# Kernel tuning notes

Hardware: AMD Instinct MI355X
Metric: run time of the kernel (lower is better)

The kernel has to match this reference:

```python
import jax, jax.numpy as jnp
import numpy as np

N = 8192
D_IN = 128
D_OUT = 128


def setup_inputs() -> dict:
    key = jax.random.key(0)
    k1, k2, k3 = jax.random.split(key, 3)
    node_features = jax.random.normal(k1, (N, D_IN), dtype=jnp.float32)
    adj_matrix = jax.random.uniform(k2, (N, N), dtype=jnp.float32)
    # Xavier-uniform weight, zero bias (as in reset_parameters)
    limit = float(np.sqrt(6.0 / (D_IN + D_OUT)))
    weight = jax.random.uniform(k3, (D_IN, D_OUT), dtype=jnp.float32,
                                minval=-limit, maxval=limit)
    bias = jnp.zeros((D_OUT,), dtype=jnp.float32)
    return {"node_features": node_features, "adj_matrix": adj_matrix,
            "weight": weight, "bias": bias}


def reference(node_features, adj_matrix, weight, bias):
    n = adj_matrix.shape[0]
    # A_hat = A + I
    a_hat = adj_matrix + jnp.eye(n, dtype=adj_matrix.dtype)
    d_hat = jnp.sum(a_hat, axis=1)  # [N]
    # pow(d, -0.5) with inf (d==0) masked to 0
    d_inv_sqrt = jnp.where(d_hat > 0, jax.lax.rsqrt(d_hat), 0.0)
    # diag(d) @ A_hat @ diag(d) == row/col broadcast scaling (same math)
    adj_normalized = d_inv_sqrt[:, None] * a_hat * d_inv_sqrt[None, :]
    support = node_features @ weight  # [N, D_OUT]
    out = adj_normalized @ support + bias
    return out
```

## Files before the change

### kernel.cpp

```cpp
#include <hip/hip_runtime.h>

#define NN 8192
#define DD 128

typedef short s16x4 __attribute__((ext_vector_type(4)));
typedef short s16x8 __attribute__((ext_vector_type(8)));
typedef float f32x4 __attribute__((ext_vector_type(4)));
typedef unsigned short u16;
typedef const void __attribute__((address_space(1))) gvoid;
typedef void __attribute__((address_space(3))) lvoid;

__device__ __forceinline__ u16 f2bf(float f) {
  unsigned int u = __float_as_uint(f);
  u += 0x7fffu + ((u >> 16) & 1u);
  return (u16)(u >> 16);
}
__device__ __forceinline__ float bf2f(u16 h) {
  return __uint_as_float(((unsigned int)h) << 16);
}

__global__ __launch_bounds__(256) void k_prep(const float* __restrict__ A,
                                              float* __restrict__ dinv,
                                              u16* __restrict__ Abf) {
  const int row = blockIdx.x;
  const float4* Ar = (const float4*)(A + (size_t)row * NN);
  ushort4* Br = (ushort4*)(Abf + (size_t)row * NN);
  const int t = threadIdx.x;
  float s = 0.f;
#pragma unroll
  for (int i = 0; i < 8; ++i) {
    float4 v = Ar[t + 256 * i];
    s += (v.x + v.y) + (v.z + v.w);
    ushort4 b;
    b.x = f2bf(v.x); b.y = f2bf(v.y); b.z = f2bf(v.z); b.w = f2bf(v.w);
    Br[t + 256 * i] = b;
  }
#pragma unroll
  for (int off = 32; off > 0; off >>= 1) s += __shfl_down(s, off, 64);
  __shared__ float red[4];
  if ((t & 63) == 0) red[t >> 6] = s;
  __syncthreads();
  if (t == 0) {
    float d = 1.0f + ((red[0] + red[1]) + (red[2] + red[3]));
    dinv[row] = d > 0.f ? rsqrtf(d) : 0.f;
  }
}

__global__ __launch_bounds__(256) void k_support(const float* __restrict__ X,
                                                 const float* __restrict__ W,
                                                 const float* __restrict__ dinv,
                                                 u16* __restrict__ tT) {
  __shared__ __align__(16) u16 Wt[128][136];
  __shared__ __align__(16) u16 Xs[32][136];
  const int t = threadIdx.x;
  const int j0 = blockIdx.x * 32;

  const float4* W4 = (const float4*)W;
#pragma unroll
  for (int s = 0; s < 16; ++s) {
    int c = t + 256 * s;
    int k = c >> 5, n4 = c & 31;
    float4 wv = W4[c];
    Wt[n4 * 4 + 0][k] = f2bf(wv.x);
    Wt[n4 * 4 + 1][k] = f2bf(wv.y);
    Wt[n4 * 4 + 2][k] = f2bf(wv.z);
    Wt[n4 * 4 + 3][k] = f2bf(wv.w);
  }
  const float4* X4 = (const float4*)(X + (size_t)j0 * DD);
#pragma unroll
  for (int s = 0; s < 4; ++s) {
    int c = t + 256 * s;
    int j = c >> 5, q = c & 31;
    float4 xv = X4[c];
    s16x4 p;
    p[0] = (short)f2bf(xv.x); p[1] = (short)f2bf(xv.y);
    p[2] = (short)f2bf(xv.z); p[3] = (short)f2bf(xv.w);
    *(s16x4*)&Xs[j][q * 4] = p;
  }
  __syncthreads();

  const int w = t >> 6, L = t & 63, lrow = L & 15, quad = L >> 4;
  f32x4 acc[2][2] = {};
#pragma unroll
  for (int ks = 0; ks < 4; ++ks) {
    const int k = ks * 32;
    s16x8 fa[2], fb[2];
#pragma unroll
    for (int nt = 0; nt < 2; ++nt)
      fa[nt] = *(const s16x8*)&Wt[w * 32 + nt * 16 + lrow][k + quad * 8];
#pragma unroll
    for (int jt = 0; jt < 2; ++jt)
      fb[jt] = *(const s16x8*)&Xs[jt * 16 + lrow][k + quad * 8];
#pragma unroll
    for (int nt = 0; nt < 2; ++nt)
#pragma unroll
      for (int jt = 0; jt < 2; ++jt)
        acc[nt][jt] = __builtin_amdgcn_mfma_f32_16x16x32_bf16(fa[nt], fb[jt], acc[nt][jt], 0, 0, 0);
  }

#pragma unroll
  for (int jt = 0; jt < 2; ++jt) {
    const int j = j0 + jt * 16 + lrow;
    const float dv = dinv[j];
#pragma unroll
    for (int nt = 0; nt < 2; ++nt) {
#pragma unroll
      for (int r = 0; r < 4; ++r) {
        const int n = w * 32 + nt * 16 + quad * 4 + r;
        tT[(size_t)n * NN + j] = f2bf(dv * acc[nt][jt][r]);
      }
    }
  }
}

#define TILE_BYTES 20480
__global__ __launch_bounds__(256) void k_gemm(const u16* __restrict__ Abf,
                                              const u16* __restrict__ tT,
                                              float* __restrict__ part) {
  __shared__ __align__(16) unsigned char sh[2][TILE_BYTES];
  const int t = threadIdx.x;
  const int bm = blockIdx.x >> 1;
  const int kh = blockIdx.x & 1;
  const int kbase = kh * (NN / 2);
  const int w = t >> 6, L = t & 63, lrow = L & 15, quad = L >> 4;
  const size_t row0 = (size_t)bm * 32;

  auto prefetch = [&](int buf, int k0) {
#pragma unroll
    for (int j = 0; j < 5; ++j) {
      const int g = w * 5 + j;
      const int o = g * 1024 + L * 16;
      const u16* src;
      if (g < 4) {
        const int r = o >> 7, c = (o >> 4) & 7;
        src = Abf + (row0 + r) * NN + (k0 + ((c ^ (r & 7)) << 3));
      } else {
        const int o2 = o - 4096;
        const int r = o2 >> 7, c = (o2 >> 4) & 7;
        src = tT + (size_t)r * NN + (k0 + ((c ^ (r & 7)) << 3));
      }
      __builtin_amdgcn_global_load_lds((gvoid*)src,
                                       (lvoid*)&sh[buf][g * 1024], 16, 0, 0);
    }
  };

  f32x4 acc[2][2] = {};
  prefetch(0, kbase);
  __syncthreads();

  for (int it = 0; it < 64; ++it) {
    const int cur = it & 1;
    if (it < 63) prefetch(cur ^ 1, kbase + (it + 1) * 64);
    const unsigned char* Ab = &sh[cur][0];
    const unsigned char* Bb = &sh[cur][4096];
#pragma unroll
    for (int s = 0; s < 2; ++s) {
      const int cx = (((s * 4) | quad) ^ (lrow & 7)) << 4;
      s16x8 fa0 = *(const s16x8*)(Ab + lrow * 128 + cx);
      s16x8 fa1 = *(const s16x8*)(Ab + (16 + lrow) * 128 + cx);
      s16x8 fb0 = *(const s16x8*)(Bb + (w * 32 + lrow) * 128 + cx);
      s16x8 fb1 = *(const s16x8*)(Bb + (w * 32 + 16 + lrow) * 128 + cx);
      acc[0][0] = __builtin_amdgcn_mfma_f32_16x16x32_bf16(fa0, fb0, acc[0][0], 0, 0, 0);
      acc[0][1] = __builtin_amdgcn_mfma_f32_16x16x32_bf16(fa0, fb1, acc[0][1], 0, 0, 0);
      acc[1][0] = __builtin_amdgcn_mfma_f32_16x16x32_bf16(fa1, fb0, acc[1][0], 0, 0, 0);
      acc[1][1] = __builtin_amdgcn_mfma_f32_16x16x32_bf16(fa1, fb1, acc[1][1], 0, 0, 0);
    }
    __syncthreads();
  }

  float* pbase = part + (size_t)kh * NN * DD;
#pragma unroll
  for (int mt = 0; mt < 2; ++mt) {
#pragma unroll
    for (int r = 0; r < 4; ++r) {
      const int i = (int)row0 + mt * 16 + quad * 4 + r;
#pragma unroll
      for (int nt = 0; nt < 2; ++nt) {
        const int n = w * 32 + nt * 16 + lrow;
        pbase[(size_t)i * DD + n] = acc[mt][nt][r];
      }
    }
  }
}

__global__ __launch_bounds__(256) void k_reduce(const float* __restrict__ part,
                                                const u16* __restrict__ tT,
                                                const float* __restrict__ dinv,
                                                const float* __restrict__ bias,
                                                float* __restrict__ out) {
  const int gid = blockIdx.x * 256 + threadIdx.x;
  const int i = gid >> 5;
  const int c = gid & 31;
  const float4 p0 = ((const float4*)part)[(size_t)i * 32 + c];
  const float4 p1 = ((const float4*)(part + (size_t)NN * DD))[(size_t)i * 32 + c];
  const float4 bb = ((const float4*)bias)[c];
  const float dv = dinv[i];
  const int n = c * 4;
  float4 o;
  o.x = dv * (p0.x + p1.x + bf2f(tT[(size_t)(n + 0) * NN + i])) + bb.x;
  o.y = dv * (p0.y + p1.y + bf2f(tT[(size_t)(n + 1) * NN + i])) + bb.y;
  o.z = dv * (p0.z + p1.z + bf2f(tT[(size_t)(n + 2) * NN + i])) + bb.z;
  o.w = dv * (p0.w + p1.w + bf2f(tT[(size_t)(n + 3) * NN + i])) + bb.w;
  ((float4*)out)[(size_t)i * 32 + c] = o;
}

extern "C" void kernel_launch(void* const* d_in, const int* in_sizes, int n_in,
                              void* d_out, int out_size, void* d_ws, size_t ws_size,
                              hipStream_t stream) {
  const float* X    = (const float*)d_in[0];
  const float* A    = (const float*)d_in[1];
  const float* W    = (const float*)d_in[2];
  const float* bias = (const float*)d_in[3];
  float* out = (float*)d_out;

  float* dinv = (float*)d_ws;
  u16*   tT   = (u16*)((char*)d_ws + 32768);
  float* part = (float*)((char*)d_ws + 32768 + 2097152);
  u16*   Abf  = (u16*)((char*)d_ws + 32768 + 2097152 + 8388608);

  hipLaunchKernelGGL(k_prep,    dim3(8192), dim3(256), 0, stream, A, dinv, Abf);
  hipLaunchKernelGGL(k_support, dim3(256),  dim3(256), 0, stream, X, W, dinv, tT);
  hipLaunchKernelGGL(k_gemm,    dim3(512),  dim3(256), 0, stream, Abf, tT, part);
  hipLaunchKernelGGL(k_reduce,  dim3(1024), dim3(256), 0, stream, part, tT, dinv, bias, out);
}
```

Before: 456.6 us.

## Drop LDS staging in GEMM and fuse reduction via atomic adds to output

The GEMM kernel no longer stages A and tT tiles through LDS with async global-to-LDS loads. Each lane now reads its MFMA fragments directly from global memory. The separate reduce kernel and the partials buffer are removed: the support kernel writes the self-loop term plus bias into out, and both K-halves of the GEMM atomically add their scaled partial sums into out. This saves a launch and the partials round trip, but the direct loads are strided rows with no reuse across waves. The atomics also make the summation order nondeterministic.

```diff
diff --git a/kernel.cpp b/kernel.cpp
--- a/kernel.cpp
+++ b/kernel.cpp
@@ -7,8 +7,6 @@
 typedef short s16x8 __attribute__((ext_vector_type(8)));
 typedef float f32x4 __attribute__((ext_vector_type(4)));
 typedef unsigned short u16;
-typedef const void __attribute__((address_space(1))) gvoid;
-typedef void __attribute__((address_space(3))) lvoid;
 
 __device__ __forceinline__ u16 f2bf(float f) {
   unsigned int u = __float_as_uint(f);
@@ -49,7 +47,9 @@
 __global__ __launch_bounds__(256) void k_support(const float* __restrict__ X,
                                                  const float* __restrict__ W,
                                                  const float* __restrict__ dinv,
-                                                 u16* __restrict__ tT) {
+                                                 const float* __restrict__ bias,
+                                                 u16* __restrict__ tT,
+                                                 float* __restrict__ out) {
   __shared__ __align__(16) u16 Wt[128][136];
   __shared__ __align__(16) u16 Xs[32][136];
   const int t = threadIdx.x;
@@ -107,101 +107,55 @@
 #pragma unroll
       for (int r = 0; r < 4; ++r) {
         const int n = w * 32 + nt * 16 + quad * 4 + r;
-        tT[(size_t)n * NN + j] = f2bf(dv * acc[nt][jt][r]);
+        const float sv = acc[nt][jt][r];
+        tT[(size_t)n * NN + j] = f2bf(dv * sv);
+        out[(size_t)j * DD + n] = dv * (dv * sv) + bias[n];
       }
     }
   }
 }
 
-#define TILE_BYTES 20480
 __global__ __launch_bounds__(256) void k_gemm(const u16* __restrict__ Abf,
                                               const u16* __restrict__ tT,
-                                              float* __restrict__ part) {
-  __shared__ __align__(16) unsigned char sh[2][TILE_BYTES];
+                                              const float* __restrict__ dinv,
+                                              float* __restrict__ out) {
   const int t = threadIdx.x;
-  const int bm = blockIdx.x >> 1;
-  const int kh = blockIdx.x & 1;
-  const int kbase = kh * (NN / 2);
   const int w = t >> 6, L = t & 63, lrow = L & 15, quad = L >> 4;
-  const size_t row0 = (size_t)bm * 32;
+  const int bm = blockIdx.x >> 1, kh = blockIdx.x & 1;
+  const int i0 = bm * 32;
+  const size_t k0 = (size_t)kh * (NN / 2);
+  const u16* A0 = Abf + (size_t)(i0 + lrow) * NN + k0 + quad * 8;
+  const u16* A1 = A0 + (size_t)16 * NN;
+  const u16* B0 = tT + (size_t)(w * 32 + lrow) * NN + k0 + quad * 8;
+  const u16* B1 = B0 + (size_t)16 * NN;
 
-  auto prefetch = [&](int buf, int k0) {
-#pragma unroll
-    for (int j = 0; j < 5; ++j) {
-      const int g = w * 5 + j;
-      const int o = g * 1024 + L * 16;
-      const u16* src;
-      if (g < 4) {
-        const int r = o >> 7, c = (o >> 4) & 7;
-        src = Abf + (row0 + r) * NN + (k0 + ((c ^ (r & 7)) << 3));
-      } else {
-        const int o2 = o - 4096;
-        const int r = o2 >> 7, c = (o2 >> 4) & 7;
-        src = tT + (size_t)r * NN + (k0 + ((c ^ (r & 7)) << 3));
-      }
-      __builtin_amdgcn_global_load_lds((gvoid*)src,
-                                       (lvoid*)&sh[buf][g * 1024], 16, 0, 0);
-    }
-  };
-
-  f32x4 acc[2][2] = {};
-  prefetch(0, kbase);
-  __syncthreads();
-
-  for (int it = 0; it < 64; ++it) {
-    const int cur = it & 1;
-    if (it < 63) prefetch(cur ^ 1, kbase + (it + 1) * 64);
-    const unsigned char* Ab = &sh[cur][0];
-    const unsigned char* Bb = &sh[cur][4096];
-#pragma unroll
-    for (int s = 0; s < 2; ++s) {
-      const int cx = (((s * 4) | quad) ^ (lrow & 7)) << 4;
-      s16x8 fa0 = *(const s16x8*)(Ab + lrow * 128 + cx);
-      s16x8 fa1 = *(const s16x8*)(Ab + (16 + lrow) * 128 + cx);
-      s16x8 fb0 = *(const s16x8*)(Bb + (w * 32 + lrow) * 128 + cx);
-      s16x8 fb1 = *(const s16x8*)(Bb + (w * 32 + 16 + lrow) * 128 + cx);
-      acc[0][0] = __builtin_amdgcn_mfma_f32_16x16x32_bf16(fa0, fb0, acc[0][0], 0, 0, 0);
-      acc[0][1] = __builtin_amdgcn_mfma_f32_16x16x32_bf16(fa0, fb1, acc[0][1], 0, 0, 0);
-      acc[1][0] = __builtin_amdgcn_mfma_f32_16x16x32_bf16(fa1, fb0, acc[1][0], 0, 0, 0);
-      acc[1][1] = __builtin_amdgcn_mfma_f32_16x16x32_bf16(fa1, fb1, acc[1][1], 0, 0, 0);
-    }
-    __syncthreads();
+  f32x4 acc00 = {}, acc01 = {}, acc10 = {}, acc11 = {};
+#pragma unroll 4
+  for (int k = 0; k < NN / 2; k += 32) {
+    s16x8 fa0 = *(const s16x8*)(A0 + k);
+    s16x8 fa1 = *(const s16x8*)(A1 + k);
+    s16x8 fb0 = *(const s16x8*)(B0 + k);
+    s16x8 fb1 = *(const s16x8*)(B1 + k);
+    acc00 = __builtin_amdgcn_mfma_f32_16x16x32_bf16(fa0, fb0, acc00, 0, 0, 0);
+    acc01 = __builtin_amdgcn_mfma_f32_16x16x32_bf16(fa0, fb1, acc01, 0, 0, 0);
+    acc10 = __builtin_amdgcn_mfma_f32_16x16x32_bf16(fa1, fb0, acc10, 0, 0, 0);
+    acc11 = __builtin_amdgcn_mfma_f32_16x16x32_bf16(fa1, fb1, acc11, 0, 0, 0);
   }
 
-  float* pbase = part + (size_t)kh * NN * DD;
+  f32x4 accs[2][2] = {{acc00, acc01}, {acc10, acc11}};
 #pragma unroll
   for (int mt = 0; mt < 2; ++mt) {
 #pragma unroll
     for (int r = 0; r < 4; ++r) {
-      const int i = (int)row0 + mt * 16 + quad * 4 + r;
+      const int i = i0 + mt * 16 + quad * 4 + r;
+      const float dv = dinv[i];
 #pragma unroll
       for (int nt = 0; nt < 2; ++nt) {
         const int n = w * 32 + nt * 16 + lrow;
-        pbase[(size_t)i * DD + n] = acc[mt][nt][r];
+        unsafeAtomicAdd(&out[(size_t)i * DD + n], dv * accs[mt][nt][r]);
       }
     }
   }
-}
-
-__global__ __launch_bounds__(256) void k_reduce(const float* __restrict__ part,
-                                                const u16* __restrict__ tT,
-                                                const float* __restrict__ dinv,
-                                                const float* __restrict__ bias,
-                                                float* __restrict__ out) {
-  const int gid = blockIdx.x * 256 + threadIdx.x;
-  const int i = gid >> 5;
-  const int c = gid & 31;
-  const float4 p0 = ((const float4*)part)[(size_t)i * 32 + c];
-  const float4 p1 = ((const float4*)(part + (size_t)NN * DD))[(size_t)i * 32 + c];
-  const float4 bb = ((const float4*)bias)[c];
-  const float dv = dinv[i];
-  const int n = c * 4;
-  float4 o;
-  o.x = dv * (p0.x + p1.x + bf2f(tT[(size_t)(n + 0) * NN + i])) + bb.x;
-  o.y = dv * (p0.y + p1.y + bf2f(tT[(size_t)(n + 1) * NN + i])) + bb.y;
-  o.z = dv * (p0.z + p1.z + bf2f(tT[(size_t)(n + 2) * NN + i])) + bb.z;
-  o.w = dv * (p0.w + p1.w + bf2f(tT[(size_t)(n + 3) * NN + i])) + bb.w;
-  ((float4*)out)[(size_t)i * 32 + c] = o;
 }
 
 extern "C" void kernel_launch(void* const* d_in, const int* in_sizes, int n_in,
@@ -215,11 +169,9 @@
 
   float* dinv = (float*)d_ws;
   u16*   tT   = (u16*)((char*)d_ws + 32768);
-  float* part = (float*)((char*)d_ws + 32768 + 2097152);
-  u16*   Abf  = (u16*)((char*)d_ws + 32768 + 2097152 + 8388608);
+  u16*   Abf  = (u16*)((char*)d_ws + 32768 + 2097152);
 
   hipLaunchKernelGGL(k_prep,    dim3(8192), dim3(256), 0, stream, A, dinv, Abf);
-  hipLaunchKernelGGL(k_support, dim3(256),  dim3(256), 0, stream, X, W, dinv, tT);
-  hipLaunchKernelGGL(k_gemm,    dim3(512),  dim3(256), 0, stream, Abf, tT, part);
-  hipLaunchKernelGGL(k_reduce,  dim3(1024), dim3(256), 0, stream, part, tT, dinv, bias, out);
+  hipLaunchKernelGGL(k_support, dim3(256),  dim3(256), 0, stream, X, W, dinv, bias, tT, out);
+  hipLaunchKernelGGL(k_gemm,    dim3(512),  dim3(256), 0, stream, Abf, tT, dinv, out);
 }
```

New measurement: 500.2 us. 1.1x slower.

## Enlarge GEMM row tile to 64 and split K four ways

Applied to the files above, without the earlier changes.

The aggregation GEMM now gives each block 64 rows of A instead of 32 and splits the K dimension into four quarters instead of two, keeping the grid at 512 blocks. Each B fragment loaded from LDS now feeds twice as many MFMAs, so the support matrix is re-read from global/L2 half as often per output row. In exchange, the partial-sum buffer doubles to four slices, which adds extra fp32 write and read traffic in the reduce kernel, and shared memory per block grows.

```diff
diff --git a/kernel.cpp b/kernel.cpp
--- a/kernel.cpp
+++ b/kernel.cpp
@@ -113,29 +113,29 @@
   }
 }
 
-#define TILE_BYTES 20480
+#define TILE_BYTES 24576
 __global__ __launch_bounds__(256) void k_gemm(const u16* __restrict__ Abf,
                                               const u16* __restrict__ tT,
                                               float* __restrict__ part) {
   __shared__ __align__(16) unsigned char sh[2][TILE_BYTES];
   const int t = threadIdx.x;
-  const int bm = blockIdx.x >> 1;
-  const int kh = blockIdx.x & 1;
-  const int kbase = kh * (NN / 2);
+  const int bm = blockIdx.x >> 2;
+  const int kq = blockIdx.x & 3;
+  const int kbase = kq * (NN / 4);
   const int w = t >> 6, L = t & 63, lrow = L & 15, quad = L >> 4;
-  const size_t row0 = (size_t)bm * 32;
+  const size_t row0 = (size_t)bm * 64;
 
   auto prefetch = [&](int buf, int k0) {
 #pragma unroll
-    for (int j = 0; j < 5; ++j) {
-      const int g = w * 5 + j;
+    for (int j = 0; j < 6; ++j) {
+      const int g = w * 6 + j;
       const int o = g * 1024 + L * 16;
       const u16* src;
-      if (g < 4) {
+      if (g < 8) {
         const int r = o >> 7, c = (o >> 4) & 7;
         src = Abf + (row0 + r) * NN + (k0 + ((c ^ (r & 7)) << 3));
       } else {
-        const int o2 = o - 4096;
+        const int o2 = o - 8192;
         const int r = o2 >> 7, c = (o2 >> 4) & 7;
         src = tT + (size_t)r * NN + (k0 + ((c ^ (r & 7)) << 3));
       }
@@ -144,33 +144,33 @@
     }
   };
 
-  f32x4 acc[2][2] = {};
+  f32x4 acc[4][2] = {};
   prefetch(0, kbase);
   __syncthreads();
 
-  for (int it = 0; it < 64; ++it) {
+  for (int it = 0; it < 32; ++it) {
     const int cur = it & 1;
-    if (it < 63) prefetch(cur ^ 1, kbase + (it + 1) * 64);
+    if (it < 31) prefetch(cur ^ 1, kbase + (it + 1) * 64);
     const unsigned char* Ab = &sh[cur][0];
-    const unsigned char* Bb = &sh[cur][4096];
+    const unsigned char* Bb = &sh[cur][8192];
 #pragma unroll
     for (int s = 0; s < 2; ++s) {
       const int cx = (((s * 4) | quad) ^ (lrow & 7)) << 4;
-      s16x8 fa0 = *(const s16x8*)(Ab + lrow * 128 + cx);
-      s16x8 fa1 = *(const s16x8*)(Ab + (16 + lrow) * 128 + cx);
       s16x8 fb0 = *(const s16x8*)(Bb + (w * 32 + lrow) * 128 + cx);
       s16x8 fb1 = *(const s16x8*)(Bb + (w * 32 + 16 + lrow) * 128 + cx);
-      acc[0][0] = __builtin_amdgcn_mfma_f32_16x16x32_bf16(fa0, fb0, acc[0][0], 0, 0, 0);
-      acc[0][1] = __builtin_amdgcn_mfma_f32_16x16x32_bf16(fa0, fb1, acc[0][1], 0, 0, 0);
-      acc[1][0] = __builtin_amdgcn_mfma_f32_16x16x32_bf16(fa1, fb0, acc[1][0], 0, 0, 0);
-      acc[1][1] = __builtin_amdgcn_mfma_f32_16x16x32_bf16(fa1, fb1, acc[1][1], 0, 0, 0);
+#pragma unroll
+      for (int mt = 0; mt < 4; ++mt) {
+        s16x8 fa = *(const s16x8*)(Ab + (mt * 16 + lrow) * 128 + cx);
+        acc[mt][0] = __builtin_amdgcn_mfma_f32_16x16x32_bf16(fa, fb0, acc[mt][0], 0, 0, 0);
+        acc[mt][1] = __builtin_amdgcn_mfma_f32_16x16x32_bf16(fa, fb1, acc[mt][1], 0, 0, 0);
+      }
     }
     __syncthreads();
   }
 
-  float* pbase = part + (size_t)kh * NN * DD;
-#pragma unroll
-  for (int mt = 0; mt < 2; ++mt) {
+  float* pbase = part + (size_t)kq * NN * DD;
+#pragma unroll
+  for (int mt = 0; mt < 4; ++mt) {
 #pragma unroll
     for (int r = 0; r < 4; ++r) {
       const int i = (int)row0 + mt * 16 + quad * 4 + r;
@@ -191,17 +191,20 @@
   const int gid = blockIdx.x * 256 + threadIdx.x;
   const int i = gid >> 5;
   const int c = gid & 31;
-  const float4 p0 = ((const float4*)part)[(size_t)i * 32 + c];
-  const float4 p1 = ((const float4*)(part + (size_t)NN * DD))[(size_t)i * 32 + c];
+  const size_t idx = (size_t)i * 32 + c;
+  const float4 p0 = ((const float4*)part)[idx];
+  const float4 p1 = ((const float4*)(part + (size_t)NN * DD))[idx];
+  const float4 p2 = ((const float4*)(part + (size_t)2 * NN * DD))[idx];
+  const float4 p3 = ((const float4*)(part + (size_t)3 * NN * DD))[idx];
   const float4 bb = ((const float4*)bias)[c];
   const float dv = dinv[i];
   const int n = c * 4;
   float4 o;
-  o.x = dv * (p0.x + p1.x + bf2f(tT[(size_t)(n + 0) * NN + i])) + bb.x;
-  o.y = dv * (p0.y + p1.y + bf2f(tT[(size_t)(n + 1) * NN + i])) + bb.y;
-  o.z = dv * (p0.z + p1.z + bf2f(tT[(size_t)(n + 2) * NN + i])) + bb.z;
-  o.w = dv * (p0.w + p1.w + bf2f(tT[(size_t)(n + 3) * NN + i])) + bb.w;
-  ((float4*)out)[(size_t)i * 32 + c] = o;
+  o.x = dv * (((p0.x + p1.x) + (p2.x + p3.x)) + bf2f(tT[(size_t)(n + 0) * NN + i])) + bb.x;
+  o.y = dv * (((p0.y + p1.y) + (p2.y + p3.y)) + bf2f(tT[(size_t)(n + 1) * NN + i])) + bb.y;
+  o.z = dv * (((p0.z + p1.z) + (p2.z + p3.z)) + bf2f(tT[(size_t)(n + 2) * NN + i])) + bb.z;
+  o.w = dv * (((p0.w + p1.w) + (p2.w + p3.w)) + bf2f(tT[(size_t)(n + 3) * NN + i])) + bb.w;
+  ((float4*)out)[idx] = o;
 }
 
 extern "C" void kernel_launch(void* const* d_in, const int* in_sizes, int n_in,
@@ -216,7 +219,7 @@
   float* dinv = (float*)d_ws;
   u16*   tT   = (u16*)((char*)d_ws + 32768);
   float* part = (float*)((char*)d_ws + 32768 + 2097152);
-  u16*   Abf  = (u16*)((char*)d_ws + 32768 + 2097152 + 8388608);
+  u16*   Abf  = (u16*)((char*)d_ws + 32768 + 2097152 + 16777216);
 
   hipLaunchKernelGGL(k_prep,    dim3(8192), dim3(256), 0, stream, A, dinv, Abf);
   hipLaunchKernelGGL(k_support, dim3(256),  dim3(256), 0, stream, X, W, dinv, tT);
```

Result: faster. 439.1 us (-3.8%).
